# Performance work log

Hardware: AMD Instinct MI355X
Metric: run time of the kernel (lower is better)

The kernel has to match this reference:

```python
import jax, jax.numpy as jnp
import numpy as np

B, D, E, H, T = 16384, 1024, 8, 512, 256
NUM_TASKS = 3  # purchase, quality, price


def setup_inputs() -> dict:
    key = jax.random.key(0)
    ks = jax.random.split(key, 12)
    s_in = 1.0 / np.sqrt(D)
    s_h = 1.0 / np.sqrt(H)
    s_t = 1.0 / np.sqrt(T)
    return {
        "x": jax.random.normal(ks[0], (B, D), dtype=jnp.float32),
        # expert layer 1: [E, D, H], layer 2: [E, H, H]
        "We1": jax.random.uniform(ks[1], (E, D, H), jnp.float32, -s_in, s_in),
        "be1": jax.random.uniform(ks[2], (E, H), jnp.float32, -s_in, s_in),
        "We2": jax.random.uniform(ks[3], (E, H, H), jnp.float32, -s_h, s_h),
        "be2": jax.random.uniform(ks[4], (E, H), jnp.float32, -s_h, s_h),
        # gates (one per task): [T_tasks, D, E]
        "Wg": jax.random.uniform(ks[5], (NUM_TASKS, D, E), jnp.float32, -s_in, s_in),
        "bg": jax.random.uniform(ks[6], (NUM_TASKS, E), jnp.float32, -s_in, s_in),
        # towers: [T_tasks, H, T] then [T_tasks, T, 1]
        "Wt1": jax.random.uniform(ks[7], (NUM_TASKS, H, T), jnp.float32, -s_h, s_h),
        "bt1": jax.random.uniform(ks[8], (NUM_TASKS, T), jnp.float32, -s_h, s_h),
        "Wt2": jax.random.uniform(ks[9], (NUM_TASKS, T, 1), jnp.float32, -s_t, s_t),
        "bt2": jax.random.uniform(ks[10], (NUM_TASKS, 1), jnp.float32, -s_t, s_t),
    }


def reference(x, We1, be1, We2, be2, Wg, bg, Wt1, bt1, Wt2, bt2):
    # Batched expert MLPs (dropout = identity in eval): [B, E, H]
    h1 = jax.nn.relu(jnp.einsum("bd,edh->beh", x, We1) + be1)
    expert_out = jax.nn.relu(jnp.einsum("beh,ehk->bek", h1, We2) + be2)
    # Per-task softmax gates: [T, B, E]
    gates = jax.nn.softmax(jnp.einsum("bd,tde->tbe", x, Wg) + bg[:, None, :], axis=-1)
    # Weighted combine: [T, B, H]
    task_in = jnp.einsum("tbe,beh->tbh", gates, expert_out)
    # Towers: [T, B, 1]
    th = jax.nn.relu(jnp.einsum("tbh,thk->tbk", task_in, Wt1) + bt1[:, None, :])
    preds = jax.nn.sigmoid(jnp.einsum("tbk,tko->tbo", th, Wt2) + bt2[:, None, :])
    return (preds[0], preds[1], preds[2])
```

## Files before the change

kernel.cpp:

```cpp
#include <hip/hip_runtime.h>


#define BM 128
#define BN 128
#define BK 64

typedef __attribute__((ext_vector_type(8))) short short8;
typedef __attribute__((ext_vector_type(4))) float floatx4;
typedef __attribute__((ext_vector_type(4))) unsigned short ushortx4;
typedef __attribute__((ext_vector_type(8))) unsigned short ushortx8;

__device__ __forceinline__ unsigned short f32_to_bf16(float f) {
  unsigned int u = __float_as_uint(f);
  u += 0x7fffu + ((u >> 16) & 1u);
  return (unsigned short)(u >> 16);
}
__device__ __forceinline__ float bf16_to_f32(unsigned short h) {
  return __uint_as_float(((unsigned int)h) << 16);
}

__device__ __forceinline__ void async_cp16(const void* g, void* lds) {
  __builtin_amdgcn_global_load_lds(
      (const __attribute__((address_space(1))) void*)g,
      (__attribute__((address_space(3))) void*)lds, 16, 0, 0);
}

__device__ __forceinline__ void transpose_slice(
    const float* __restrict__ in, unsigned short* __restrict__ out,
    int K, int N, float (*tile)[33]) {
  int n0 = blockIdx.x * 32, k0 = blockIdx.y * 32;
  for (int i = threadIdx.y; i < 32; i += 8)
    tile[i][threadIdx.x] = in[(size_t)(k0 + i) * N + n0 + threadIdx.x];
  __syncthreads();
  for (int i = threadIdx.y; i < 32; i += 8)
    out[(size_t)(n0 + i) * K + k0 + threadIdx.x] = f32_to_bf16(tile[threadIdx.x][i]);
}

__global__ void prep_kernel(const float* __restrict__ We1, const float* __restrict__ We2,
                            const float* __restrict__ Wt1, const float* __restrict__ Wg,
                            unsigned short* __restrict__ W1T, unsigned short* __restrict__ W2T,
                            unsigned short* __restrict__ Wt1T, float* __restrict__ WgT) {
  __shared__ float tile[32][33];
  int z = blockIdx.z;
  if (z < 8) {
    transpose_slice(We1 + (size_t)z * 524288, W1T + (size_t)z * 524288, 1024, 512, tile);
  } else if (z < 16) {
    if (blockIdx.y < 16)
      transpose_slice(We2 + (size_t)(z - 8) * 262144, W2T + (size_t)(z - 8) * 262144, 512, 512, tile);
  } else if (z < 19) {
    if (blockIdx.x < 8 && blockIdx.y < 16)
      transpose_slice(Wt1 + (size_t)(z - 16) * 131072, Wt1T + (size_t)(z - 16) * 131072, 512, 256, tile);
  } else {
    if (blockIdx.x < 16 && blockIdx.y < 6) {
      int idx = (blockIdx.y * 16 + blockIdx.x) * 256 + threadIdx.y * 32 + threadIdx.x;
      int t = idx >> 13, r = idx & 8191, e = r >> 10, d = r & 1023;
      WgT[idx] = Wg[t * 8192 + d * 8 + e];
    }
  }
}

__global__ __launch_bounds__(256) void gates_cvt_kernel(
    const float* __restrict__ x, const float* __restrict__ WgT,
    const float* __restrict__ bg, float* __restrict__ gout,
    unsigned short* __restrict__ xb) {
  int wave = threadIdx.x >> 6, lane = threadIdx.x & 63;
  int b = blockIdx.x * 4 + wave;
  const float* xr = x + (size_t)b * 1024;
  float xv[16];
#pragma unroll
  for (int j = 0; j < 16; j++) xv[j] = xr[lane + 64 * j];
  unsigned short* xbr = xb + (size_t)b * 1024;
#pragma unroll
  for (int j = 0; j < 16; j++) xbr[lane + 64 * j] = f32_to_bf16(xv[j]);
  float mylogit = 0.f;
#pragma unroll
  for (int te = 0; te < 24; te++) {
    const float* w = WgT + te * 1024;
    float a = 0.f;
#pragma unroll
    for (int j = 0; j < 16; j++) a += xv[j] * w[lane + 64 * j];
#pragma unroll
    for (int off = 32; off > 0; off >>= 1) a += __shfl_xor(a, off, 64);
    if (lane == te) mylogit = a;
  }
  if (lane < 24) {
    int t = lane >> 3, e = lane & 7;
    float logit = mylogit + bg[lane];
    float m = logit;
    m = fmaxf(m, __shfl_xor(m, 4, 64));
    m = fmaxf(m, __shfl_xor(m, 2, 64));
    m = fmaxf(m, __shfl_xor(m, 1, 64));
    float ex = __expf(logit - m);
    float s = ex;
    s += __shfl_xor(s, 4, 64);
    s += __shfl_xor(s, 2, 64);
    s += __shfl_xor(s, 1, 64);
    gout[(size_t)t * 131072 + (size_t)b * 8 + e] = ex / s;
  }
}

__global__ __launch_bounds__(256) void gemm_bt_relu(
    const unsigned short* __restrict__ Abase, long aOffZ, int lda,
    const unsigned short* __restrict__ Bbase, long bOffZ,
    const float* __restrict__ biasBase, int biasOffZ,
    unsigned short* __restrict__ Cbase, long cOffZ, int ldc,
    int K) {
  __shared__ __align__(16) unsigned short As[BM * BK];
  __shared__ __align__(16) unsigned short Bs[BN * BK];
  const int tid = threadIdx.x;
  const int z = blockIdx.z;
  const unsigned short* A = Abase + (size_t)aOffZ * z + (size_t)blockIdx.x * BM * lda;
  const unsigned short* Bt = Bbase + (size_t)bOffZ * z + (size_t)blockIdx.y * BN * K;
  const float* bias = biasBase + (size_t)biasOffZ * z + blockIdx.y * BN;
  unsigned short* C = Cbase + (size_t)cOffZ * z + (size_t)blockIdx.x * BM * ldc + blockIdx.y * BN;

  const int wave = tid >> 6, lane = tid & 63;
  const int wm = (wave >> 1) * 64, wn = (wave & 1) * 64;
  const int lm = lane & 15, lq = lane >> 4;
  const int sw = lm & 7;

  floatx4 acc[4][4] = {};

  const int sr = tid >> 3;
  const int sc = (((tid & 7) ^ (sr & 7)) << 3);

  for (int kt = 0; kt < K; kt += BK) {
#pragma unroll
    for (int i = 0; i < 4; i++)
      async_cp16(A + (size_t)(sr + 32 * i) * lda + kt + sc,
                 (char*)As + i * 4096 + tid * 16);
#pragma unroll
    for (int i = 0; i < 4; i++)
      async_cp16(Bt + (size_t)(sr + 32 * i) * K + kt + sc,
                 (char*)Bs + i * 4096 + tid * 16);
    __syncthreads();
#pragma unroll
    for (int ks = 0; ks < 2; ks++) {
      short8 af[4], bf[4];
      const int ch = ((ks * 4 + lq) ^ sw) << 3;
#pragma unroll
      for (int i = 0; i < 4; i++)
        af[i] = *(const short8*)(As + (wm + 16 * i + lm) * BK + ch);
#pragma unroll
      for (int j = 0; j < 4; j++)
        bf[j] = *(const short8*)(Bs + (wn + 16 * j + lm) * BK + ch);
#pragma unroll
      for (int i = 0; i < 4; i++)
#pragma unroll
        for (int j = 0; j < 4; j++)
          acc[i][j] = __builtin_amdgcn_mfma_f32_16x16x32_bf16(af[i], bf[j], acc[i][j], 0, 0, 0);
    }
    __syncthreads();
  }

#pragma unroll
  for (int i = 0; i < 4; i++) {
    const int row = wm + 16 * i + lq * 4;
#pragma unroll
    for (int j = 0; j < 4; j++) {
      const int col = wn + 16 * j + lm;
      const float bv = bias[col];
#pragma unroll
      for (int v = 0; v < 4; v++) {
        float val = fmaxf(acc[i][j][v] + bv, 0.0f);
        C[(size_t)(row + v) * ldc + col] = f32_to_bf16(val);
      }
    }
  }
}


#define STAGE_A256(buf, half, tt) do {                                       \
    const int kt_ = ((tt) < NT ? (tt) : 0) << 6;                             \
    _Pragma("unroll") for (int g_ = 0; g_ < 2; ++g_) {                       \
      const int rb_ = ((half) + 2 * g_) * 64;                                \
      async_cp16(A + (size_t)(rb_ + sr) * lda + kt_ + sc,                    \
                 (char*)As + (buf) * 32768 + rb_ * 128 + tid * 16);          \
    } } while (0)

#define STAGE_B256(buf, half, tt) do {                                       \
    const int kt_ = ((tt) < NT ? (tt) : 0) << 6;                             \
    _Pragma("unroll") for (int g_ = 0; g_ < 2; ++g_) {                       \
      const int rb_ = (half) * 128 + g_ * 64;                                \
      async_cp16(Bt + (size_t)(rb_ + sr) * K + kt_ + sc,                     \
                 (char*)Bs + (buf) * 32768 + rb_ * 128 + tid * 16);          \
    } } while (0)

#define DS_A256(mi, ks)                                                      \
  (*(const short8*)(As + cur * 16384 + (wm + 16 * (mi) + lm) * 64 +          \
                    ((((ks) * 4 + lq) ^ sw) << 3)))
#define DS_B256(nj, ks)                                                      \
  (*(const short8*)(Bs + cur * 16384 + (wn + 16 * (nj) + lm) * 64 +          \
                    ((((ks) * 4 + lq) ^ sw) << 3)))

#define PHASE256(p, STAGE_STMT, ENDWAIT) do {                                \
    short8 af[2][2];                                                         \
    af[0][0] = DS_A256(2 * (p) + 0, 0); af[0][1] = DS_A256(2 * (p) + 0, 1);  \
    af[1][0] = DS_A256(2 * (p) + 1, 0); af[1][1] = DS_A256(2 * (p) + 1, 1);  \
    if ((p) == 0) {                                                          \
      _Pragma("unroll") for (int nj = 0; nj < 4; ++nj) {                     \
        bf[nj][0] = DS_B256(nj, 0); bf[nj][1] = DS_B256(nj, 1);              \
      }                                                                      \
    }                                                                        \
    STAGE_STMT;                                                              \
    __builtin_amdgcn_s_barrier();                                            \
    asm volatile("s_waitcnt lgkmcnt(0)" ::: "memory");                       \
    __builtin_amdgcn_sched_barrier(0);                                       \
    __builtin_amdgcn_s_setprio(1);                                           \
    _Pragma("unroll") for (int d_ = 0; d_ < 2; ++d_)                         \
      _Pragma("unroll") for (int nj = 0; nj < 4; ++nj)                       \
        _Pragma("unroll") for (int ks = 0; ks < 2; ++ks)                     \
          acc[2 * (p) + d_][nj] = __builtin_amdgcn_mfma_f32_16x16x32_bf16(   \
              af[d_][ks], bf[nj][ks], acc[2 * (p) + d_][nj], 0, 0, 0);       \
    __builtin_amdgcn_s_setprio(0);                                           \
    if (ENDWAIT) asm volatile("s_waitcnt vmcnt(6)" ::: "memory");            \
    __builtin_amdgcn_s_barrier();                                            \
  } while (0)

__global__ __launch_bounds__(512) void gemm256_bt_relu(
    const unsigned short* __restrict__ Abase, long aOffZ, int lda,
    const unsigned short* __restrict__ Bbase, long bOffZ,
    const float* __restrict__ biasBase, int biasOffZ,
    unsigned short* __restrict__ Cbase, long cOffZ, int ldc,
    int K) {
  __shared__ __align__(16) unsigned short As[2 * 256 * 64];
  __shared__ __align__(16) unsigned short Bs[2 * 256 * 64];
  const int tid = threadIdx.x;
  const int z = blockIdx.z;
  const unsigned short* A = Abase + (size_t)aOffZ * z + (size_t)blockIdx.x * 256 * lda;
  const unsigned short* Bt = Bbase + (size_t)bOffZ * z + (size_t)blockIdx.y * 256 * K;
  const float* bias = biasBase + (size_t)biasOffZ * z + blockIdx.y * 256;
  unsigned short* C = Cbase + (size_t)cOffZ * z + (size_t)blockIdx.x * 256 * ldc + blockIdx.y * 256;

  const int wave = tid >> 6, lane = tid & 63;
  const int wm = (wave >> 2) * 128, wn = (wave & 3) * 64;
  const int lm = lane & 15, lq = lane >> 4;
  const int sw = lm & 7;
  const int sr = tid >> 3;
  const int sc = (((tid & 7) ^ (sr & 7)) << 3);
  const int NT = K >> 6;

  floatx4 acc[8][4] = {};
  short8 bf[4][2];

  STAGE_A256(0, 0, 0); STAGE_A256(0, 1, 0); STAGE_B256(0, 0, 0); STAGE_B256(0, 1, 0);
  asm volatile("s_waitcnt vmcnt(4)" ::: "memory");
  STAGE_B256(1, 0, 1); STAGE_A256(1, 0, 1); STAGE_B256(1, 1, 1);
  asm volatile("s_waitcnt vmcnt(6)" ::: "memory");
  __builtin_amdgcn_s_barrier();

  for (int t = 0; t < NT; ++t) {
    const int cur = t & 1;
    PHASE256(0, STAGE_A256(cur ^ 1, 1, t + 1), 0);
    PHASE256(1, STAGE_B256(cur, 0, t + 2), 0);
    PHASE256(2, STAGE_A256(cur, 0, t + 2), 0);
    PHASE256(3, STAGE_B256(cur, 1, t + 2), 1);
  }

  asm volatile("s_waitcnt vmcnt(0)" ::: "memory");

  float bv[4];
#pragma unroll
  for (int nj = 0; nj < 4; ++nj) bv[nj] = bias[wn + 16 * nj + lm];
#pragma unroll
  for (int mi = 0; mi < 8; ++mi) {
    const int row = wm + 16 * mi + lq * 4;
#pragma unroll
    for (int nj = 0; nj < 4; ++nj) {
      const int col = wn + 16 * nj + lm;
#pragma unroll
      for (int v = 0; v < 4; ++v) {
        float val = fmaxf(acc[mi][nj][v] + bv[nj], 0.0f);
        C[(size_t)(row + v) * ldc + col] = f32_to_bf16(val);
      }
    }
  }
}

__global__ void combine_kernel(const unsigned short* __restrict__ eo,
                               const float* __restrict__ gates,
                               unsigned short* __restrict__ ti,
                               int b0, int Bc) {
  int tid = blockIdx.x * 256 + threadIdx.x;
  int bl = tid >> 6;
  int hc = (tid & 63) << 3;
  float g[3][8];
#pragma unroll
  for (int t = 0; t < 3; t++) {
    const floatx4* gp = (const floatx4*)(gates + ((size_t)t * 16384 + b0 + bl) * 8);
    floatx4 g0 = gp[0], g1 = gp[1];
#pragma unroll
    for (int j = 0; j < 4; j++) { g[t][j] = g0[j]; g[t][4 + j] = g1[j]; }
  }
  float out[3][8] = {};
#pragma unroll
  for (int e = 0; e < 8; e++) {
    ushortx8 v = *(const ushortx8*)(eo + ((size_t)bl * 8 + e) * 512 + hc);
#pragma unroll
    for (int j = 0; j < 8; j++) {
      float f = bf16_to_f32(v[j]);
#pragma unroll
      for (int t = 0; t < 3; t++) out[t][j] += g[t][e] * f;
    }
  }
#pragma unroll
  for (int t = 0; t < 3; t++) {
    ushortx8 o;
#pragma unroll
    for (int j = 0; j < 8; j++) o[j] = f32_to_bf16(out[t][j]);
    *(ushortx8*)(ti + ((size_t)t * Bc + bl) * 512 + hc) = o;
  }
}

__global__ __launch_bounds__(512) void tower_fused_kernel(
    const unsigned short* __restrict__ tic, const unsigned short* __restrict__ Wt1T,
    const float* __restrict__ bt1, const float* __restrict__ Wt2,
    const float* __restrict__ bt2, float* __restrict__ out,
    int b0, int Bc) {
  __shared__ __align__(16) unsigned short As[128 * 64];
  __shared__ __align__(16) unsigned short Bs[256 * 64];
  const int tid = threadIdx.x;
  const int mtiles = Bc >> 7;
  const int t = blockIdx.x / mtiles;
  const int xbl = blockIdx.x % mtiles;
  const unsigned short* A = tic + ((size_t)t * Bc + (size_t)xbl * 128) * 512;
  const unsigned short* Bt = Wt1T + (size_t)t * 131072;

  const int wave = tid >> 6, lane = tid & 63;
  const int wm = (wave >> 2) * 64, wn = (wave & 3) * 64;
  const int lm = lane & 15, lq = lane >> 4;
  const int sw = lm & 7;

  floatx4 acc[4][4] = {};

  const int sr = tid >> 3;
  const int sc = (((tid & 7) ^ (sr & 7)) << 3);

  for (int kt = 0; kt < 512; kt += 64) {
#pragma unroll
    for (int i = 0; i < 2; i++)
      async_cp16(A + (size_t)(sr + 64 * i) * 512 + kt + sc,
                 (char*)As + i * 8192 + tid * 16);
#pragma unroll
    for (int i = 0; i < 4; i++)
      async_cp16(Bt + (size_t)(sr + 64 * i) * 512 + kt + sc,
                 (char*)Bs + i * 8192 + tid * 16);
    __syncthreads();
#pragma unroll
    for (int ks = 0; ks < 2; ks++) {
      short8 af[4], bf[4];
      const int ch = ((ks * 4 + lq) ^ sw) << 3;
#pragma unroll
      for (int i = 0; i < 4; i++)
        af[i] = *(const short8*)(As + (wm + 16 * i + lm) * 64 + ch);
#pragma unroll
      for (int j = 0; j < 4; j++)
        bf[j] = *(const short8*)(Bs + (wn + 16 * j + lm) * 64 + ch);
#pragma unroll
      for (int i = 0; i < 4; i++)
#pragma unroll
        for (int j = 0; j < 4; j++)
          acc[i][j] = __builtin_amdgcn_mfma_f32_16x16x32_bf16(af[i], bf[j], acc[i][j], 0, 0, 0);
    }
    __syncthreads();
  }

  float b1v[4], w2v[4];
#pragma unroll
  for (int j = 0; j < 4; j++) {
    int col = wn + 16 * j + lm;
    b1v[j] = bt1[t * 256 + col];
    w2v[j] = Wt2[t * 256 + col];
  }
  float* pt = (float*)As;
#pragma unroll
  for (int i = 0; i < 4; i++) {
#pragma unroll
    for (int v = 0; v < 4; v++) {
      float p = 0.f;
#pragma unroll
      for (int j = 0; j < 4; j++)
        p += fmaxf(acc[i][j][v] + b1v[j], 0.0f) * w2v[j];
      p += __shfl_xor(p, 1, 64);
      p += __shfl_xor(p, 2, 64);
      p += __shfl_xor(p, 4, 64);
      p += __shfl_xor(p, 8, 64);
      if (lm == 0) pt[(wm + 16 * i + lq * 4 + v) * 4 + (wave & 3)] = p;
    }
  }
  __syncthreads();
  if (tid < 128) {
    float s = pt[tid * 4] + pt[tid * 4 + 1] + pt[tid * 4 + 2] + pt[tid * 4 + 3] + bt2[t];
    out[(t << 14) + b0 + xbl * 128 + tid] = 1.f / (1.f + __expf(-s));
  }
}

extern "C" void kernel_launch(void* const* d_in, const int* in_sizes, int n_in,
                              void* d_out, int out_size, void* d_ws, size_t ws_size,
                              hipStream_t stream) {
  (void)in_sizes; (void)n_in; (void)out_size;
  const float* x   = (const float*)d_in[0];
  const float* We1 = (const float*)d_in[1];
  const float* be1 = (const float*)d_in[2];
  const float* We2 = (const float*)d_in[3];
  const float* be2 = (const float*)d_in[4];
  const float* Wg  = (const float*)d_in[5];
  const float* bg  = (const float*)d_in[6];
  const float* Wt1 = (const float*)d_in[7];
  const float* bt1 = (const float*)d_in[8];
  const float* Wt2 = (const float*)d_in[9];
  const float* bt2 = (const float*)d_in[10];
  float* out = (float*)d_out;

  char* ws = (char*)d_ws;
  unsigned short* xb   = (unsigned short*)(ws + 0);
  unsigned short* W1T  = (unsigned short*)(ws + 33554432);
  unsigned short* W2T  = (unsigned short*)(ws + 41943040);
  unsigned short* Wt1T = (unsigned short*)(ws + 46137344);
  float*          gts  = (float*)(ws + 46923776);
  float*          WgT  = (float*)(ws + 48496640);
  const size_t fixed = 48594944;

  size_t rem = ws_size > fixed ? ws_size - fixed : 0;
  int Bc = 16384;
  while (Bc > 512 && (size_t)Bc * 19456 > rem) Bc >>= 1;
  const int nc = 16384 / Bc;

  char* cb = ws + fixed;
  unsigned short* h1c = (unsigned short*)(cb);
  unsigned short* eoc = (unsigned short*)(cb + (size_t)Bc * 8192);
  unsigned short* tic = (unsigned short*)(cb + (size_t)Bc * 16384);

  prep_kernel<<<dim3(16, 32, 20), dim3(32, 8), 0, stream>>>(We1, We2, Wt1, Wg, W1T, W2T, Wt1T, WgT);
  gates_cvt_kernel<<<4096, 256, 0, stream>>>(x, WgT, bg, gts, xb);

  for (int c = 0; c < nc; c++) {
    const unsigned short* xbc = xb + (size_t)c * Bc * 1024;
    if (Bc >= 4096) {
      gemm256_bt_relu<<<dim3(Bc / 256, 2, 8), 512, 0, stream>>>(
          xbc, 0L, 1024, W1T, 524288L, be1, 512, h1c, 512L, 4096, 1024);
      gemm256_bt_relu<<<dim3(Bc / 256, 2, 8), 512, 0, stream>>>(
          h1c, 512L, 4096, W2T, 262144L, be2, 512, eoc, 512L, 4096, 512);
    } else {
      gemm_bt_relu<<<dim3(Bc / 128, 4, 8), 256, 0, stream>>>(
          xbc, 0L, 1024, W1T, 524288L, be1, 512, h1c, 512L, 4096, 1024);
      gemm_bt_relu<<<dim3(Bc / 128, 4, 8), 256, 0, stream>>>(
          h1c, 512L, 4096, W2T, 262144L, be2, 512, eoc, 512L, 4096, 512);
    }
    combine_kernel<<<Bc / 4, 256, 0, stream>>>(eoc, gts, tic, c * Bc, Bc);
    tower_fused_kernel<<<3 * (Bc / 128), 512, 0, stream>>>(
        tic, Wt1T, bt1, Wt2, bt2, out, c * Bc, Bc);
  }
}
```

Baseline: 520.1 us.

## Software-pipeline LDS fragment reads in 256-tile GEMM; use 128-tile kernel for layer 2

Restructures the main loop of the 256x256 GEMM so LDS fragment reads for the next phase are issued before the MFMAs of the current phase. Partial lgkmcnt waits replace the full wait plus extra barrier in each phase, so LDS latency can hide behind matrix math. Separately, the second expert layer (K=512) now always uses the 128x128 GEMM kernel, which gives more blocks for the short-K problem. The change holds more fragment registers live, which may raise register pressure, and relies on the counted waits being correct.

```diff
diff --git a/kernel.cpp b/kernel.cpp
--- a/kernel.cpp
+++ b/kernel.cpp
@@ -193,28 +193,20 @@
   (*(const short8*)(Bs + cur * 16384 + (wn + 16 * (nj) + lm) * 64 +          \
                     ((((ks) * 4 + lq) ^ sw) << 3)))
 
-#define PHASE256(p, STAGE_STMT, ENDWAIT) do {                                \
-    short8 af[2][2];                                                         \
-    af[0][0] = DS_A256(2 * (p) + 0, 0); af[0][1] = DS_A256(2 * (p) + 0, 1);  \
-    af[1][0] = DS_A256(2 * (p) + 1, 0); af[1][1] = DS_A256(2 * (p) + 1, 1);  \
-    if ((p) == 0) {                                                          \
-      _Pragma("unroll") for (int nj = 0; nj < 4; ++nj) {                     \
-        bf[nj][0] = DS_B256(nj, 0); bf[nj][1] = DS_B256(nj, 1);              \
-      }                                                                      \
-    }                                                                        \
-    STAGE_STMT;                                                              \
-    __builtin_amdgcn_s_barrier();                                            \
-    asm volatile("s_waitcnt lgkmcnt(0)" ::: "memory");                       \
-    __builtin_amdgcn_sched_barrier(0);                                       \
-    __builtin_amdgcn_s_setprio(1);                                           \
+#define RD_A2(dst, mi0) do {                                                 \
+    dst[0][0] = DS_A256((mi0), 0);     dst[0][1] = DS_A256((mi0), 1);        \
+    dst[1][0] = DS_A256((mi0) + 1, 0); dst[1][1] = DS_A256((mi0) + 1, 1); } while (0)
+
+#define WAIT_LGKM(n) do {                                                    \
+    asm volatile("s_waitcnt lgkmcnt(" #n ")" ::: "memory");                  \
+    __builtin_amdgcn_sched_barrier(0); } while (0)
+
+#define MFMA16(src, q) do {                                                  \
     _Pragma("unroll") for (int d_ = 0; d_ < 2; ++d_)                         \
       _Pragma("unroll") for (int nj = 0; nj < 4; ++nj)                       \
         _Pragma("unroll") for (int ks = 0; ks < 2; ++ks)                     \
-          acc[2 * (p) + d_][nj] = __builtin_amdgcn_mfma_f32_16x16x32_bf16(   \
-              af[d_][ks], bf[nj][ks], acc[2 * (p) + d_][nj], 0, 0, 0);       \
-    __builtin_amdgcn_s_setprio(0);                                           \
-    if (ENDWAIT) asm volatile("s_waitcnt vmcnt(6)" ::: "memory");            \
-    __builtin_amdgcn_s_barrier();                                            \
+          acc[2 * (q) + d_][nj] = __builtin_amdgcn_mfma_f32_16x16x32_bf16(   \
+              src[d_][ks], bfr[nj][ks], acc[2 * (q) + d_][nj], 0, 0, 0);     \
   } while (0)
 
 __global__ __launch_bounds__(512) void gemm256_bt_relu(
@@ -241,7 +233,6 @@
   const int NT = K >> 6;
 
   floatx4 acc[8][4] = {};
-  short8 bf[4][2];
 
   STAGE_A256(0, 0, 0); STAGE_A256(0, 1, 0); STAGE_B256(0, 0, 0); STAGE_B256(0, 1, 0);
   asm volatile("s_waitcnt vmcnt(4)" ::: "memory");
@@ -251,10 +242,52 @@
 
   for (int t = 0; t < NT; ++t) {
     const int cur = t & 1;
-    PHASE256(0, STAGE_A256(cur ^ 1, 1, t + 1), 0);
-    PHASE256(1, STAGE_B256(cur, 0, t + 2), 0);
-    PHASE256(2, STAGE_A256(cur, 0, t + 2), 0);
-    PHASE256(3, STAGE_B256(cur, 1, t + 2), 1);
+    short8 afA[2][2], afB[2][2], bfr[4][2];
+    RD_A2(afA, 0);
+    bfr[0][0] = DS_B256(0, 0); bfr[1][0] = DS_B256(1, 0);
+    bfr[2][0] = DS_B256(2, 0); bfr[3][0] = DS_B256(3, 0);
+    STAGE_A256(cur ^ 1, 1, t + 1);
+    bfr[0][1] = DS_B256(0, 1); bfr[1][1] = DS_B256(1, 1);
+    bfr[2][1] = DS_B256(2, 1); bfr[3][1] = DS_B256(3, 1);
+    RD_A2(afB, 2);
+    WAIT_LGKM(8);
+    __builtin_amdgcn_s_setprio(1);
+#pragma unroll
+    for (int d_ = 0; d_ < 2; ++d_)
+#pragma unroll
+      for (int nj = 0; nj < 4; ++nj)
+        acc[d_][nj] = __builtin_amdgcn_mfma_f32_16x16x32_bf16(
+            afA[d_][0], bfr[nj][0], acc[d_][nj], 0, 0, 0);
+    WAIT_LGKM(4);
+#pragma unroll
+    for (int d_ = 0; d_ < 2; ++d_)
+#pragma unroll
+      for (int nj = 0; nj < 4; ++nj)
+        acc[d_][nj] = __builtin_amdgcn_mfma_f32_16x16x32_bf16(
+            afA[d_][1], bfr[nj][1], acc[d_][nj], 0, 0, 0);
+    __builtin_amdgcn_s_setprio(0);
+    __builtin_amdgcn_s_barrier();
+    STAGE_B256(cur, 0, t + 2);
+    RD_A2(afA, 4);
+    WAIT_LGKM(4);
+    __builtin_amdgcn_s_setprio(1);
+    MFMA16(afB, 1);
+    __builtin_amdgcn_s_setprio(0);
+    __builtin_amdgcn_s_barrier();
+    STAGE_A256(cur, 0, t + 2);
+    RD_A2(afB, 6);
+    WAIT_LGKM(4);
+    __builtin_amdgcn_s_setprio(1);
+    MFMA16(afA, 2);
+    __builtin_amdgcn_s_setprio(0);
+    __builtin_amdgcn_s_barrier();
+    STAGE_B256(cur, 1, t + 2);
+    WAIT_LGKM(0);
+    __builtin_amdgcn_s_setprio(1);
+    MFMA16(afB, 3);
+    __builtin_amdgcn_s_setprio(0);
+    asm volatile("s_waitcnt vmcnt(6)" ::: "memory");
+    __builtin_amdgcn_s_barrier();
   }
 
   asm volatile("s_waitcnt vmcnt(0)" ::: "memory");
@@ -439,14 +472,12 @@
     if (Bc >= 4096) {
       gemm256_bt_relu<<<dim3(Bc / 256, 2, 8), 512, 0, stream>>>(
           xbc, 0L, 1024, W1T, 524288L, be1, 512, h1c, 512L, 4096, 1024);
-      gemm256_bt_relu<<<dim3(Bc / 256, 2, 8), 512, 0, stream>>>(
-          h1c, 512L, 4096, W2T, 262144L, be2, 512, eoc, 512L, 4096, 512);
     } else {
       gemm_bt_relu<<<dim3(Bc / 128, 4, 8), 256, 0, stream>>>(
           xbc, 0L, 1024, W1T, 524288L, be1, 512, h1c, 512L, 4096, 1024);
-      gemm_bt_relu<<<dim3(Bc / 128, 4, 8), 256, 0, stream>>>(
-          h1c, 512L, 4096, W2T, 262144L, be2, 512, eoc, 512L, 4096, 512);
-    }
+    }
+    gemm_bt_relu<<<dim3(Bc / 128, 4, 8), 256, 0, stream>>>(
+        h1c, 512L, 4096, W2T, 262144L, be2, 512, eoc, 512L, 4096, 512);
     combine_kernel<<<Bc / 4, 256, 0, stream>>>(eoc, gts, tic, c * Bc, Bc);
     tower_fused_kernel<<<3 * (Bc / 128), 512, 0, stream>>>(
         tic, Wt1T, bt1, Wt2, bt2, out, c * Bc, Bc);
```

Result: faster. 505.8 us (-2.7%).
